# Performance work log

Hardware: AMD Instinct MI355X
Metric: run time of the kernel (lower is better)

Reference implementation:

```python
import jax, jax.numpy as jnp
import numpy as np

B, S, E, H, V, C = 64, 512, 256, 128, 50000, 2


def setup_inputs() -> dict:
    key = jax.random.key(0)
    ks = jax.random.split(key, 12)
    sentences = jax.random.randint(ks[0], (B, S), 0, V, dtype=jnp.int32)
    # sparse binary adjacency (dependency-tree-like), float for bmm
    adj = (jax.random.uniform(ks[1], (B, S, S)) < 0.05).astype(jnp.float32)
    emb_table = jax.random.normal(ks[2], (V, E), dtype=jnp.float32) * 0.02
    W1 = jax.random.normal(ks[3], (H, E), dtype=jnp.float32) * 0.05
    b1 = jnp.zeros((H,), jnp.float32)
    W2 = jax.random.normal(ks[4], (H, H), dtype=jnp.float32) * 0.05
    b2 = jnp.zeros((H,), jnp.float32)
    W3 = jax.random.normal(ks[5], (H, H), dtype=jnp.float32) * 0.05
    b3 = jnp.zeros((H,), jnp.float32)
    Wp = jax.random.normal(ks[6], (C, H), dtype=jnp.float32) * 0.05
    bp = jnp.zeros((C,), jnp.float32)
    return {"sentences": sentences, "adj": adj, "emb_table": emb_table,
            "W1": W1, "b1": b1, "W2": W2, "b2": b2, "W3": W3, "b3": b3,
            "Wp": Wp, "bp": bp}


def reference(sentences, adj, emb_table, W1, b1, W2, b2, W3, b3, Wp, bp):
    # embedding lookup (dropout is eval-mode identity)
    h = emb_table[sentences]  # [B, S, E]
    # degree normalization term (self-loop adds +1)
    deg = jnp.sum(adj, axis=-1, keepdims=True) + 1.0  # [B, S, 1]
    for W, b in ((W1, b1), (W2, b2), (W3, b3)):
        agg = jnp.einsum('bst,btd->bsd', adj, h)  # bmm(adj, h)
        # layer(agg) + layer(h) == (agg + h) @ W^T + 2b  (shared weights)
        h = ((agg + h) @ W.T + 2.0 * b) / deg
        h = jax.nn.relu(h)
    # AdaptiveMaxPool1d(1) over sequence dim
    pooled = jnp.max(h, axis=1)  # [B, H]
    logits = pooled @ Wp.T + bp  # [B, C]
    return logits
```

## Files before the change

### kernel.cpp

```cpp
#include <hip/hip_runtime.h>
#include <hip/hip_bf16.h>

typedef unsigned short ushort_t;

#define B_ 64
#define S_ 512
#define E_ 256
#define H_ 128
#define M_ (B_ * S_)
#define CAP_ 128


template <int K, bool GATHER, bool ADJ>
__global__ __launch_bounds__(256, 2) void k_gemm(const float* __restrict__ X,
                                                 const int* __restrict__ sent,
                                                 const float* __restrict__ emb,
                                                 const float* __restrict__ W,
                                                 float* __restrict__ out,
                                                 const float* __restrict__ adj,
                                                 ushort_t* __restrict__ idxl,
                                                 int* __restrict__ nnz,
                                                 float* __restrict__ invdeg) {
    __shared__ float Ws[128 * 68];
    __shared__ float Xs[4][16 * 36];
    int tid  = threadIdx.x;
    int wave = tid >> 6, lane = tid & 63;
    int rb      = blockIdx.x >> 1;
    int colBase = (blockIdx.x & 1) * 64;
    int rowBase = rb * 128 + wave * 32;

    int cc = lane & 15, rr = lane >> 4;
    int kg = lane & 3,  rowi = lane >> 2;

    const float* xs0;
    const float* xs1;
    if (GATHER) {
        xs0 = emb + (size_t)sent[rowBase + rowi]      * K + kg * 4;
        xs1 = emb + (size_t)sent[rowBase + rowi + 16] * K + kg * 4;
    } else {
        xs0 = X + (size_t)(rowBase + rowi)      * K + kg * 4;
        xs1 = X + (size_t)(rowBase + rowi + 16) * K + kg * 4;
    }

    float acc[8][4] = {};
    float* xsw = Xs[wave];

    for (int kh = 0; kh < K; kh += 128) {
        if (kh) __syncthreads();
        {
            int j  = tid & 63;
            int kq = tid >> 6;
            const float* wp = W + (size_t)(colBase + j) * K + kh + kq * 32;
            #pragma unroll
            for (int i = 0; i < 8; ++i) {
                float4 v = *(const float4*)(wp + i * 4);
                int k = kq * 32 + i * 4;
                Ws[(k + 0) * 68 + j] = v.x; Ws[(k + 1) * 68 + j] = v.y;
                Ws[(k + 2) * 68 + j] = v.z; Ws[(k + 3) * 68 + j] = v.w;
            }
        }
        float4 f0 = *(const float4*)(xs0 + kh);
        float4 f1 = *(const float4*)(xs1 + kh);
        __syncthreads();

        #pragma unroll 1
        for (int kk = 0; kk < 128; kk += 16) {
            xsw[(kg * 4 + 0) * 36 + rowi] = f0.x;
            xsw[(kg * 4 + 1) * 36 + rowi] = f0.y;
            xsw[(kg * 4 + 2) * 36 + rowi] = f0.z;
            xsw[(kg * 4 + 3) * 36 + rowi] = f0.w;
            xsw[(kg * 4 + 0) * 36 + rowi + 16] = f1.x;
            xsw[(kg * 4 + 1) * 36 + rowi + 16] = f1.y;
            xsw[(kg * 4 + 2) * 36 + rowi + 16] = f1.z;
            xsw[(kg * 4 + 3) * 36 + rowi + 16] = f1.w;
            if (kk + 16 < 128) {
                f0 = *(const float4*)(xs0 + kh + kk + 16);
                f1 = *(const float4*)(xs1 + kh + kk + 16);
            }
            #pragma unroll
            for (int k = 0; k < 16; ++k) {
                float4 a0 = *(const float4*)&xsw[k * 36 + rr * 8];
                float4 a1 = *(const float4*)&xsw[k * 36 + rr * 8 + 4];
                float4 wv = *(const float4*)&Ws[(kk + k) * 68 + cc * 4];
                float xv[8] = {a0.x, a0.y, a0.z, a0.w, a1.x, a1.y, a1.z, a1.w};
                #pragma unroll
                for (int i = 0; i < 8; ++i) {
                    acc[i][0] += xv[i] * wv.x;
                    acc[i][1] += xv[i] * wv.y;
                    acc[i][2] += xv[i] * wv.z;
                    acc[i][3] += xv[i] * wv.w;
                }
            }
        }
    }

    #pragma unroll
    for (int i = 0; i < 8; ++i) {
        int row = rowBase + rr * 8 + i;
        float4 o = {acc[i][0], acc[i][1], acc[i][2], acc[i][3]};
        *(float4*)(out + (size_t)row * H_ + colBase + cc * 4) = o;
    }

    if (ADJ) {
        #pragma unroll 1
        for (int it = 0; it < 16; ++it) {
            int row = blockIdx.x * 64 + it * 4 + wave;
            const float4* arow = (const float4*)(adj + (size_t)row * S_);
            ushort_t* dst = idxl + (size_t)row * CAP_;
            int total = 0;
            #pragma unroll
            for (int c = 0; c < 2; ++c) {
                float4 v = arow[c * 64 + lane];
                float f[4] = {v.x, v.y, v.z, v.w};
                #pragma unroll
                for (int j = 0; j < 4; ++j) {
                    unsigned long long m = __ballot(f[j] != 0.0f);
                    if (f[j] != 0.0f) {
                        int pos = total + __popcll(m & ((1ull << lane) - 1ull));
                        if (pos < CAP_) dst[pos] = (ushort_t)(c * 256 + lane * 4 + j);
                    }
                    total += __popcll(m);
                }
            }
            if (lane == 0) {
                nnz[row] = total < CAP_ ? total : CAP_;
                invdeg[row] = 1.0f / (float)(total + 1);
            }
        }
    }
}

template <bool POOL>
__global__ __launch_bounds__(256) void k_aggf(const float* __restrict__ Y,
                                              const ushort_t* __restrict__ idxl,
                                              const int* __restrict__ nnz,
                                              const float* __restrict__ invdeg,
                                              const float* __restrict__ bias,
                                              float* __restrict__ out) {
    int x    = blockIdx.x;
    int xcd  = x & 7;
    int slot = x >> 3;
    int b    = xcd + 8 * (slot >> 6);
    int g    = slot & 63;
    int r    = threadIdx.x >> 5;
    int row  = b * S_ + g * 8 + r;
    int c    = threadIdx.x & 31;

    const float4* Y4 = (const float4*)Y;
    int n = nnz[row];
    const ushort_t* il = idxl + (size_t)row * CAP_;
    float4 acc = Y4[(size_t)row * 32 + c];
    float4 acc2 = {0.f, 0.f, 0.f, 0.f};
    size_t base = (size_t)b * S_ * 32;

    int i = 0;
    for (; i + 4 <= n; i += 4) {
        int t0 = il[i], t1 = il[i + 1], t2 = il[i + 2], t3 = il[i + 3];
        float4 v0 = Y4[base + (size_t)t0 * 32 + c];
        float4 v1 = Y4[base + (size_t)t1 * 32 + c];
        float4 v2 = Y4[base + (size_t)t2 * 32 + c];
        float4 v3 = Y4[base + (size_t)t3 * 32 + c];
        acc.x += v0.x + v1.x; acc.y += v0.y + v1.y;
        acc.z += v0.z + v1.z; acc.w += v0.w + v1.w;
        acc2.x += v2.x + v3.x; acc2.y += v2.y + v3.y;
        acc2.z += v2.z + v3.z; acc2.w += v2.w + v3.w;
    }
    for (; i < n; ++i) {
        int t = il[i];
        float4 v = Y4[base + (size_t)t * 32 + c];
        acc.x += v.x; acc.y += v.y; acc.z += v.z; acc.w += v.w;
    }
    acc.x += acc2.x; acc.y += acc2.y; acc.z += acc2.z; acc.w += acc2.w;

    float inv = invdeg[row];
    float4 bv = ((const float4*)bias)[c];
    float4 o;
    o.x = fmaxf((acc.x + 2.0f * bv.x) * inv, 0.0f);
    o.y = fmaxf((acc.y + 2.0f * bv.y) * inv, 0.0f);
    o.z = fmaxf((acc.z + 2.0f * bv.z) * inv, 0.0f);
    o.w = fmaxf((acc.w + 2.0f * bv.w) * inv, 0.0f);

    if (!POOL) {
        ((float4*)out)[(size_t)row * 32 + c] = o;
    } else {
        __shared__ float4 sm[8][33];
        sm[r][c] = o;
        __syncthreads();
        if (r == 0) {
            float4 m = sm[0][c];
            #pragma unroll
            for (int q = 1; q < 8; ++q) {
                float4 v = sm[q][c];
                m.x = fmaxf(m.x, v.x); m.y = fmaxf(m.y, v.y);
                m.z = fmaxf(m.z, v.z); m.w = fmaxf(m.w, v.w);
            }
            ((float4*)out)[((size_t)b * 64 + g) * 32 + c] = m;
        }
    }
}

__global__ void k_final(const float* __restrict__ pp,
                        const float* __restrict__ Wp,
                        const float* __restrict__ bp,
                        float* __restrict__ out) {
    int b = blockIdx.x, j = threadIdx.x;
    const float* p = pp + (size_t)b * 64 * H_ + j;
    float m = -1e30f;
    #pragma unroll 8
    for (int i = 0; i < 64; ++i) m = fmaxf(m, p[(size_t)i * H_]);
    float t0 = m * Wp[j];
    float t1 = m * Wp[H_ + j];
    #pragma unroll
    for (int off = 32; off > 0; off >>= 1) {
        t0 += __shfl_down(t0, off);
        t1 += __shfl_down(t1, off);
    }
    __shared__ float red[2][2];
    int wave = j >> 6, lane = j & 63;
    if (lane == 0) { red[0][wave] = t0; red[1][wave] = t1; }
    __syncthreads();
    if (j == 0) out[b * 2 + 0] = red[0][0] + red[0][1] + bp[0];
    if (j == 1) out[b * 2 + 1] = red[1][0] + red[1][1] + bp[1];
}

extern "C" void kernel_launch(void* const* d_in, const int* in_sizes, int n_in,
                              void* d_out, int out_size, void* d_ws, size_t ws_size,
                              hipStream_t stream) {
    const int*   sent = (const int*)d_in[0];
    const float* adj  = (const float*)d_in[1];
    const float* emb  = (const float*)d_in[2];
    const float* W1   = (const float*)d_in[3];
    const float* b1   = (const float*)d_in[4];
    const float* W2   = (const float*)d_in[5];
    const float* b2   = (const float*)d_in[6];
    const float* W3   = (const float*)d_in[7];
    const float* b3   = (const float*)d_in[8];
    const float* Wp   = (const float*)d_in[9];
    const float* bp   = (const float*)d_in[10];
    float* out = (float*)d_out;

    char* ws = (char*)d_ws;
    float*    Ybuf   = (float*)ws;
    float*    h1     = (float*)(ws + ((size_t)16 << 20));
    float*    h2     = (float*)(ws + ((size_t)32 << 20));
    char*     base   = ws + ((size_t)48 << 20);
    float*    invdeg = (float*)base;
    int*      nnz    = (int*)(base + (size_t)M_ * 4);
    ushort_t* idxl   = (ushort_t*)(base + (size_t)M_ * 8);
    float*    pp     = (float*)(base + (size_t)M_ * 8 + (size_t)M_ * CAP_ * 2);

    k_gemm<E_, true, true><<<512, 256, 0, stream>>>(nullptr, sent, emb, W1, Ybuf,
                                                    adj, idxl, nnz, invdeg);
    k_aggf<false><<<M_ / 8, 256, 0, stream>>>(Ybuf, idxl, nnz, invdeg, b1, h1);

    k_gemm<H_, false, false><<<512, 256, 0, stream>>>(h1, nullptr, nullptr, W2, Ybuf,
                                                      nullptr, nullptr, nullptr, nullptr);
    k_aggf<false><<<M_ / 8, 256, 0, stream>>>(Ybuf, idxl, nnz, invdeg, b2, h2);

    k_gemm<H_, false, false><<<512, 256, 0, stream>>>(h2, nullptr, nullptr, W3, Ybuf,
                                                      nullptr, nullptr, nullptr, nullptr);
    k_aggf<true ><<<M_ / 8, 256, 0, stream>>>(Ybuf, idxl, nnz, invdeg, b3, pp);

    k_final<<<B_, H_, 0, stream>>>(pp, Wp, bp, out);
}
```

Before: 301.2 us.

## Split adjacency compaction into separate blocks and fuse pooling with final projection

```diff
diff --git a/kernel.cpp b/kernel.cpp
--- a/kernel.cpp
+++ b/kernel.cpp
@@ -11,100 +11,30 @@
 #define CAP_ 128
 
 
-template <int K, bool GATHER, bool ADJ>
-__global__ __launch_bounds__(256, 2) void k_gemm(const float* __restrict__ X,
-                                                 const int* __restrict__ sent,
-                                                 const float* __restrict__ emb,
-                                                 const float* __restrict__ W,
-                                                 float* __restrict__ out,
-                                                 const float* __restrict__ adj,
-                                                 ushort_t* __restrict__ idxl,
-                                                 int* __restrict__ nnz,
-                                                 float* __restrict__ invdeg) {
+__global__ __launch_bounds__(256, 2) void k_g1adj(const int* __restrict__ sent,
+                                                  const float* __restrict__ emb,
+                                                  const float* __restrict__ W,
+                                                  float* __restrict__ Yout,
+                                                  const float* __restrict__ adj,
+                                                  ushort_t* __restrict__ idxl,
+                                                  int* __restrict__ nnz,
+                                                  float* __restrict__ invdeg,
+                                                  float* __restrict__ pooled,
+                                                  int* __restrict__ counter) {
     __shared__ float Ws[128 * 68];
     __shared__ float Xs[4][16 * 36];
     int tid  = threadIdx.x;
     int wave = tid >> 6, lane = tid & 63;
-    int rb      = blockIdx.x >> 1;
-    int colBase = (blockIdx.x & 1) * 64;
-    int rowBase = rb * 128 + wave * 32;
-
-    int cc = lane & 15, rr = lane >> 4;
-    int kg = lane & 3,  rowi = lane >> 2;
-
-    const float* xs0;
-    const float* xs1;
-    if (GATHER) {
-        xs0 = emb + (size_t)sent[rowBase + rowi]      * K + kg * 4;
-        xs1 = emb + (size_t)sent[rowBase + rowi + 16] * K + kg * 4;
-    } else {
-        xs0 = X + (size_t)(rowBase + rowi)      * K + kg * 4;
-        xs1 = X + (size_t)(rowBase + rowi + 16) * K + kg * 4;
-    }
-
-    float acc[8][4] = {};
-    float* xsw = Xs[wave];
-
-    for (int kh = 0; kh < K; kh += 128) {
-        if (kh) __syncthreads();
-        {
-            int j  = tid & 63;
-            int kq = tid >> 6;
-            const float* wp = W + (size_t)(colBase + j) * K + kh + kq * 32;
-            #pragma unroll
-            for (int i = 0; i < 8; ++i) {
-                float4 v = *(const float4*)(wp + i * 4);
-                int k = kq * 32 + i * 4;
-                Ws[(k + 0) * 68 + j] = v.x; Ws[(k + 1) * 68 + j] = v.y;
-                Ws[(k + 2) * 68 + j] = v.z; Ws[(k + 3) * 68 + j] = v.w;
-            }
-        }
-        float4 f0 = *(const float4*)(xs0 + kh);
-        float4 f1 = *(const float4*)(xs1 + kh);
-        __syncthreads();
-
-        #pragma unroll 1
-        for (int kk = 0; kk < 128; kk += 16) {
-            xsw[(kg * 4 + 0) * 36 + rowi] = f0.x;
-            xsw[(kg * 4 + 1) * 36 + rowi] = f0.y;
-            xsw[(kg * 4 + 2) * 36 + rowi] = f0.z;
-            xsw[(kg * 4 + 3) * 36 + rowi] = f0.w;
-            xsw[(kg * 4 + 0) * 36 + rowi + 16] = f1.x;
-            xsw[(kg * 4 + 1) * 36 + rowi + 16] = f1.y;
-            xsw[(kg * 4 + 2) * 36 + rowi + 16] = f1.z;
-            xsw[(kg * 4 + 3) * 36 + rowi + 16] = f1.w;
-            if (kk + 16 < 128) {
-                f0 = *(const float4*)(xs0 + kh + kk + 16);
-                f1 = *(const float4*)(xs1 + kh + kk + 16);
-            }
-            #pragma unroll
-            for (int k = 0; k < 16; ++k) {
-                float4 a0 = *(const float4*)&xsw[k * 36 + rr * 8];
-                float4 a1 = *(const float4*)&xsw[k * 36 + rr * 8 + 4];
-                float4 wv = *(const float4*)&Ws[(kk + k) * 68 + cc * 4];
-                float xv[8] = {a0.x, a0.y, a0.z, a0.w, a1.x, a1.y, a1.z, a1.w};
-                #pragma unroll
-                for (int i = 0; i < 8; ++i) {
-                    acc[i][0] += xv[i] * wv.x;
-                    acc[i][1] += xv[i] * wv.y;
-                    acc[i][2] += xv[i] * wv.z;
-                    acc[i][3] += xv[i] * wv.w;
-                }
-            }
-        }
-    }
-
-    #pragma unroll
-    for (int i = 0; i < 8; ++i) {
-        int row = rowBase + rr * 8 + i;
-        float4 o = {acc[i][0], acc[i][1], acc[i][2], acc[i][3]};
-        *(float4*)(out + (size_t)row * H_ + colBase + cc * 4) = o;
-    }
-
-    if (ADJ) {
+
+    if (blockIdx.x & 1) {
+        int gblk = blockIdx.x >> 1;
+        if (gblk == 0) {
+            for (int i = tid; i < B_ * H_; i += 256) pooled[i] = 0.0f;
+            if (tid == 0) *counter = 0;
+        }
         #pragma unroll 1
         for (int it = 0; it < 16; ++it) {
-            int row = blockIdx.x * 64 + it * 4 + wave;
+            int row = gblk * 64 + it * 4 + wave;
             const float4* arow = (const float4*)(adj + (size_t)row * S_);
             ushort_t* dst = idxl + (size_t)row * CAP_;
             int total = 0;
@@ -127,10 +57,156 @@
                 invdeg[row] = 1.0f / (float)(total + 1);
             }
         }
-    }
-}
-
-template <bool POOL>
+        return;
+    }
+
+    constexpr int K = E_;
+    int g       = blockIdx.x >> 1;
+    int rb      = g >> 1;
+    int colBase = (g & 1) * 64;
+    int rowBase = rb * 128 + wave * 32;
+
+    int cc = lane & 15, rr = lane >> 4;
+    int kg = lane & 3,  rowi = lane >> 2;
+
+    const float* xs0 = emb + (size_t)sent[rowBase + rowi]      * K + kg * 4;
+    const float* xs1 = emb + (size_t)sent[rowBase + rowi + 16] * K + kg * 4;
+
+    float acc[8][4] = {};
+    float* xsw = Xs[wave];
+
+    for (int kh = 0; kh < K; kh += 128) {
+        if (kh) __syncthreads();
+        {
+            int j  = tid & 63;
+            int kq = tid >> 6;
+            const float* wp = W + (size_t)(colBase + j) * K + kh + kq * 32;
+            #pragma unroll
+            for (int i = 0; i < 8; ++i) {
+                float4 v = *(const float4*)(wp + i * 4);
+                int k = kq * 32 + i * 4;
+                Ws[(k + 0) * 68 + j] = v.x; Ws[(k + 1) * 68 + j] = v.y;
+                Ws[(k + 2) * 68 + j] = v.z; Ws[(k + 3) * 68 + j] = v.w;
+            }
+        }
+        float4 f0 = *(const float4*)(xs0 + kh);
+        float4 f1 = *(const float4*)(xs1 + kh);
+        __syncthreads();
+
+        #pragma unroll 1
+        for (int kk = 0; kk < 128; kk += 16) {
+            xsw[(kg * 4 + 0) * 36 + rowi] = f0.x;
+            xsw[(kg * 4 + 1) * 36 + rowi] = f0.y;
+            xsw[(kg * 4 + 2) * 36 + rowi] = f0.z;
+            xsw[(kg * 4 + 3) * 36 + rowi] = f0.w;
+            xsw[(kg * 4 + 0) * 36 + rowi + 16] = f1.x;
+            xsw[(kg * 4 + 1) * 36 + rowi + 16] = f1.y;
+            xsw[(kg * 4 + 2) * 36 + rowi + 16] = f1.z;
+            xsw[(kg * 4 + 3) * 36 + rowi + 16] = f1.w;
+            if (kk + 16 < 128) {
+                f0 = *(const float4*)(xs0 + kh + kk + 16);
+                f1 = *(const float4*)(xs1 + kh + kk + 16);
+            }
+            #pragma unroll
+            for (int k = 0; k < 16; ++k) {
+                float4 a0 = *(const float4*)&xsw[k * 36 + rr * 8];
+                float4 a1 = *(const float4*)&xsw[k * 36 + rr * 8 + 4];
+                float4 wv = *(const float4*)&Ws[(kk + k) * 68 + cc * 4];
+                float xv[8] = {a0.x, a0.y, a0.z, a0.w, a1.x, a1.y, a1.z, a1.w};
+                #pragma unroll
+                for (int i = 0; i < 8; ++i) {
+                    acc[i][0] += xv[i] * wv.x;
+                    acc[i][1] += xv[i] * wv.y;
+                    acc[i][2] += xv[i] * wv.z;
+                    acc[i][3] += xv[i] * wv.w;
+                }
+            }
+        }
+    }
+
+    #pragma unroll
+    for (int i = 0; i < 8; ++i) {
+        int row = rowBase + rr * 8 + i;
+        float4 o = {acc[i][0], acc[i][1], acc[i][2], acc[i][3]};
+        *(float4*)(Yout + (size_t)row * H_ + colBase + cc * 4) = o;
+    }
+}
+
+__global__ __launch_bounds__(256, 2) void k_gemm(const float* __restrict__ X,
+                                                 const float* __restrict__ W,
+                                                 float* __restrict__ out) {
+    constexpr int K = H_;
+    __shared__ float Ws[128 * 68];
+    __shared__ float Xs[4][16 * 36];
+    int tid  = threadIdx.x;
+    int wave = tid >> 6, lane = tid & 63;
+    int rb      = blockIdx.x >> 1;
+    int colBase = (blockIdx.x & 1) * 64;
+    int rowBase = rb * 128 + wave * 32;
+
+    int cc = lane & 15, rr = lane >> 4;
+    int kg = lane & 3,  rowi = lane >> 2;
+
+    const float* xs0 = X + (size_t)(rowBase + rowi)      * K + kg * 4;
+    const float* xs1 = X + (size_t)(rowBase + rowi + 16) * K + kg * 4;
+
+    float acc[8][4] = {};
+    float* xsw = Xs[wave];
+
+    {
+        int j  = tid & 63;
+        int kq = tid >> 6;
+        const float* wp = W + (size_t)(colBase + j) * K + kq * 32;
+        #pragma unroll
+        for (int i = 0; i < 8; ++i) {
+            float4 v = *(const float4*)(wp + i * 4);
+            int k = kq * 32 + i * 4;
+            Ws[(k + 0) * 68 + j] = v.x; Ws[(k + 1) * 68 + j] = v.y;
+            Ws[(k + 2) * 68 + j] = v.z; Ws[(k + 3) * 68 + j] = v.w;
+        }
+    }
+    float4 f0 = *(const float4*)(xs0);
+    float4 f1 = *(const float4*)(xs1);
+    __syncthreads();
+
+    #pragma unroll 1
+    for (int kk = 0; kk < 128; kk += 16) {
+        xsw[(kg * 4 + 0) * 36 + rowi] = f0.x;
+        xsw[(kg * 4 + 1) * 36 + rowi] = f0.y;
+        xsw[(kg * 4 + 2) * 36 + rowi] = f0.z;
+        xsw[(kg * 4 + 3) * 36 + rowi] = f0.w;
+        xsw[(kg * 4 + 0) * 36 + rowi + 16] = f1.x;
+        xsw[(kg * 4 + 1) * 36 + rowi + 16] = f1.y;
+        xsw[(kg * 4 + 2) * 36 + rowi + 16] = f1.z;
+        xsw[(kg * 4 + 3) * 36 + rowi + 16] = f1.w;
+        if (kk + 16 < 128) {
+            f0 = *(const float4*)(xs0 + kk + 16);
+            f1 = *(const float4*)(xs1 + kk + 16);
+        }
+        #pragma unroll
+        for (int k = 0; k < 16; ++k) {
+            float4 a0 = *(const float4*)&xsw[k * 36 + rr * 8];
+            float4 a1 = *(const float4*)&xsw[k * 36 + rr * 8 + 4];
+            float4 wv = *(const float4*)&Ws[(kk + k) * 68 + cc * 4];
+            float xv[8] = {a0.x, a0.y, a0.z, a0.w, a1.x, a1.y, a1.z, a1.w};
+            #pragma unroll
+            for (int i = 0; i < 8; ++i) {
+                acc[i][0] += xv[i] * wv.x;
+                acc[i][1] += xv[i] * wv.y;
+                acc[i][2] += xv[i] * wv.z;
+                acc[i][3] += xv[i] * wv.w;
+            }
+        }
+    }
+
+    #pragma unroll
+    for (int i = 0; i < 8; ++i) {
+        int row = rowBase + rr * 8 + i;
+        float4 o = {acc[i][0], acc[i][1], acc[i][2], acc[i][3]};
+        *(float4*)(out + (size_t)row * H_ + colBase + cc * 4) = o;
+    }
+}
+
 __global__ __launch_bounds__(256) void k_aggf(const float* __restrict__ Y,
                                               const ushort_t* __restrict__ idxl,
                                               const int* __restrict__ nnz,
@@ -179,48 +255,107 @@
     o.y = fmaxf((acc.y + 2.0f * bv.y) * inv, 0.0f);
     o.z = fmaxf((acc.z + 2.0f * bv.z) * inv, 0.0f);
     o.w = fmaxf((acc.w + 2.0f * bv.w) * inv, 0.0f);
-
-    if (!POOL) {
-        ((float4*)out)[(size_t)row * 32 + c] = o;
-    } else {
-        __shared__ float4 sm[8][33];
-        sm[r][c] = o;
-        __syncthreads();
-        if (r == 0) {
-            float4 m = sm[0][c];
-            #pragma unroll
-            for (int q = 1; q < 8; ++q) {
-                float4 v = sm[q][c];
-                m.x = fmaxf(m.x, v.x); m.y = fmaxf(m.y, v.y);
-                m.z = fmaxf(m.z, v.z); m.w = fmaxf(m.w, v.w);
-            }
-            ((float4*)out)[((size_t)b * 64 + g) * 32 + c] = m;
-        }
-    }
-}
-
-__global__ void k_final(const float* __restrict__ pp,
-                        const float* __restrict__ Wp,
-                        const float* __restrict__ bp,
-                        float* __restrict__ out) {
-    int b = blockIdx.x, j = threadIdx.x;
-    const float* p = pp + (size_t)b * 64 * H_ + j;
-    float m = -1e30f;
-    #pragma unroll 8
-    for (int i = 0; i < 64; ++i) m = fmaxf(m, p[(size_t)i * H_]);
-    float t0 = m * Wp[j];
-    float t1 = m * Wp[H_ + j];
-    #pragma unroll
-    for (int off = 32; off > 0; off >>= 1) {
-        t0 += __shfl_down(t0, off);
-        t1 += __shfl_down(t1, off);
-    }
-    __shared__ float red[2][2];
-    int wave = j >> 6, lane = j & 63;
-    if (lane == 0) { red[0][wave] = t0; red[1][wave] = t1; }
+    ((float4*)out)[(size_t)row * 32 + c] = o;
+}
+
+__global__ __launch_bounds__(256) void k_aggp(const float* __restrict__ Y,
+                                              const ushort_t* __restrict__ idxl,
+                                              const int* __restrict__ nnz,
+                                              const float* __restrict__ invdeg,
+                                              const float* __restrict__ bias,
+                                              float* __restrict__ pooled,
+                                              int* __restrict__ counter,
+                                              const float* __restrict__ Wp,
+                                              const float* __restrict__ bp,
+                                              float* __restrict__ out) {
+    int x    = blockIdx.x;
+    int xcd  = x & 7;
+    int slot = x >> 3;
+    int b    = xcd + 8 * (slot >> 6);
+    int g    = slot & 63;
+    int r    = threadIdx.x >> 5;
+    int row  = b * S_ + g * 8 + r;
+    int c    = threadIdx.x & 31;
+
+    const float4* Y4 = (const float4*)Y;
+    int n = nnz[row];
+    const ushort_t* il = idxl + (size_t)row * CAP_;
+    float4 acc = Y4[(size_t)row * 32 + c];
+    float4 acc2 = {0.f, 0.f, 0.f, 0.f};
+    size_t base = (size_t)b * S_ * 32;
+
+    int i = 0;
+    for (; i + 4 <= n; i += 4) {
+        int t0 = il[i], t1 = il[i + 1], t2 = il[i + 2], t3 = il[i + 3];
+        float4 v0 = Y4[base + (size_t)t0 * 32 + c];
+        float4 v1 = Y4[base + (size_t)t1 * 32 + c];
+        float4 v2 = Y4[base + (size_t)t2 * 32 + c];
+        float4 v3 = Y4[base + (size_t)t3 * 32 + c];
+        acc.x += v0.x + v1.x; acc.y += v0.y + v1.y;
+        acc.z += v0.z + v1.z; acc.w += v0.w + v1.w;
+        acc2.x += v2.x + v3.x; acc2.y += v2.y + v3.y;
+        acc2.z += v2.z + v3.z; acc2.w += v2.w + v3.w;
+    }
+    for (; i < n; ++i) {
+        int t = il[i];
+        float4 v = Y4[base + (size_t)t * 32 + c];
+        acc.x += v.x; acc.y += v.y; acc.z += v.z; acc.w += v.w;
+    }
+    acc.x += acc2.x; acc.y += acc2.y; acc.z += acc2.z; acc.w += acc2.w;
+
+    float inv = invdeg[row];
+    float4 bv = ((const float4*)bias)[c];
+    float4 o;
+    o.x = fmaxf((acc.x + 2.0f * bv.x) * inv, 0.0f);
+    o.y = fmaxf((acc.y + 2.0f * bv.y) * inv, 0.0f);
+    o.z = fmaxf((acc.z + 2.0f * bv.z) * inv, 0.0f);
+    o.w = fmaxf((acc.w + 2.0f * bv.w) * inv, 0.0f);
+
+    __shared__ float4 sm[8][33];
+    sm[r][c] = o;
     __syncthreads();
-    if (j == 0) out[b * 2 + 0] = red[0][0] + red[0][1] + bp[0];
-    if (j == 1) out[b * 2 + 1] = red[1][0] + red[1][1] + bp[1];
+    if (r == 0) {
+        float4 m = sm[0][c];
+        #pragma unroll
+        for (int q = 1; q < 8; ++q) {
+            float4 v = sm[q][c];
+            m.x = fmaxf(m.x, v.x); m.y = fmaxf(m.y, v.y);
+            m.z = fmaxf(m.z, v.z); m.w = fmaxf(m.w, v.w);
+        }
+        int* pi = (int*)(pooled + (size_t)b * H_ + c * 4);
+        atomicMax(pi + 0, __float_as_int(m.x));
+        atomicMax(pi + 1, __float_as_int(m.y));
+        atomicMax(pi + 2, __float_as_int(m.z));
+        atomicMax(pi + 3, __float_as_int(m.w));
+    }
+    __syncthreads();
+
+    __shared__ int isLast;
+    if (threadIdx.x == 0) {
+        __threadfence();
+        int v = atomicAdd(counter, 1);
+        isLast = (v == gridDim.x - 1) ? 1 : 0;
+    }
+    __syncthreads();
+    if (isLast) {
+        __threadfence();
+        int t  = threadIdx.x;
+        int bb = t >> 2, q = t & 3;
+        const float* pv = pooled + (size_t)bb * H_ + q * 32;
+        float t0 = 0.f, t1 = 0.f;
+        #pragma unroll
+        for (int k = 0; k < 32; ++k) {
+            float v = pv[k];
+            t0 += v * Wp[q * 32 + k];
+            t1 += v * Wp[H_ + q * 32 + k];
+        }
+        t0 += __shfl_xor(t0, 1); t0 += __shfl_xor(t0, 2);
+        t1 += __shfl_xor(t1, 1); t1 += __shfl_xor(t1, 2);
+        if (q == 0) {
+            out[bb * 2 + 0] = t0 + bp[0];
+            out[bb * 2 + 1] = t1 + bp[1];
+        }
+    }
 }
 
 extern "C" void kernel_launch(void* const* d_in, const int* in_sizes, int n_in,
@@ -247,19 +382,17 @@
     float*    invdeg = (float*)base;
     int*      nnz    = (int*)(base + (size_t)M_ * 4);
     ushort_t* idxl   = (ushort_t*)(base + (size_t)M_ * 8);
-    float*    pp     = (float*)(base + (size_t)M_ * 8 + (size_t)M_ * CAP_ * 2);
-
-    k_gemm<E_, true, true><<<512, 256, 0, stream>>>(nullptr, sent, emb, W1, Ybuf,
-                                                    adj, idxl, nnz, invdeg);
-    k_aggf<false><<<M_ / 8, 256, 0, stream>>>(Ybuf, idxl, nnz, invdeg, b1, h1);
-
-    k_gemm<H_, false, false><<<512, 256, 0, stream>>>(h1, nullptr, nullptr, W2, Ybuf,
-                                                      nullptr, nullptr, nullptr, nullptr);
-    k_aggf<false><<<M_ / 8, 256, 0, stream>>>(Ybuf, idxl, nnz, invdeg, b2, h2);
-
-    k_gemm<H_, false, false><<<512, 256, 0, stream>>>(h2, nullptr, nullptr, W3, Ybuf,
-                                                      nullptr, nullptr, nullptr, nullptr);
-    k_aggf<true ><<<M_ / 8, 256, 0, stream>>>(Ybuf, idxl, nnz, invdeg, b3, pp);
-
-    k_final<<<B_, H_, 0, stream>>>(pp, Wp, bp, out);
-}
+    float*    pooled = (float*)(base + (size_t)M_ * 8 + (size_t)M_ * CAP_ * 2);
+    int*      counter= (int*)(base + (size_t)M_ * 8 + (size_t)M_ * CAP_ * 2 + B_ * H_ * 4);
+
+    k_g1adj<<<1024, 256, 0, stream>>>(sent, emb, W1, Ybuf,
+                                      adj, idxl, nnz, invdeg, pooled, counter);
+    k_aggf<<<M_ / 8, 256, 0, stream>>>(Ybuf, idxl, nnz, invdeg, b1, h1);
+
+    k_gemm<<<512, 256, 0, stream>>>(h1, W2, Ybuf);
+    k_aggf<<<M_ / 8, 256, 0, stream>>>(Ybuf, idxl, nnz, invdeg, b2, h2);
+
+    k_gemm<<<512, 256, 0, stream>>>(h2, W3, Ybuf);
+    k_aggp<<<M_ / 8, 256, 0, stream>>>(Ybuf, idxl, nnz, invdeg, b3,
+                                       pooled, counter, Wp, bp, out);
+}
```

After: 383.5 us. 27.3% more time.
